# Kernel optimization log

Hardware: AMD Instinct MI355X
Metric: run time of the kernel (lower is better)

The kernel has to match this reference:

```python
import jax, jax.numpy as jnp
import numpy as np

B, S, DMODEL, NHEAD = 2, 2048, 1024, 16
DK = DMODEL // NHEAD
INITRANGE = 0.1


def setup_inputs() -> dict:
    key = jax.random.key(0)
    kq, kk, kv, kwq, kwk, kwv, kwo = jax.random.split(key, 7)
    unif = lambda k, shape: jax.random.uniform(k, shape, jnp.float32, -INITRANGE, INITRANGE)
    return {
        "Q": jax.random.normal(kq, (B, S, DMODEL), jnp.float32),
        "K": jax.random.normal(kk, (B, S, DMODEL), jnp.float32),
        "V": jax.random.normal(kv, (B, S, DMODEL), jnp.float32),
        "WQ": unif(kwq, (NHEAD, DMODEL, DK)),
        "WK": unif(kwk, (NHEAD, DMODEL, DK)),
        "WV": unif(kwv, (NHEAD, DMODEL, DK)),
        "WO": unif(kwo, (NHEAD * DK, DMODEL)),
    }


def reference(Q, K, V, WQ, WK, WV, WO):
    dk = WQ.shape[-1]
    # per-head projections: [B,S,D] x [H,D,dk] -> [B,H,S,dk]
    Qi = jnp.einsum('bsd,hdk->bhsk', Q, WQ)
    Ki = jnp.einsum('bsd,hdk->bhsk', K, WK)
    Vi = jnp.einsum('bsd,hdk->bhsk', V, WV)
    scale = 1.0 / jnp.sqrt(jnp.asarray(dk, Qi.dtype))
    # full attention matrix [B,H,S,S] (faithful to the hand-rolled module; dropout in eval mode)
    attn = jax.nn.softmax(jnp.einsum('bhsk,bhtk->bhst', Qi, Ki) * scale, axis=-1)
    headi = jnp.einsum('bhst,bhtk->bhsk', attn, Vi)  # [B,H,S,dk]
    b, h, s, _ = headi.shape
    # NOTE: original does a raw reshape of contiguous (B,H,S,dk) -> (B,S,H*dk),
    # which mixes head and sequence axes in memory order. jnp row-major reshape
    # reproduces exactly the same element layout.
    out = headi.reshape(b, s, h * dk) @ WO  # [B,S,DMODEL]
    return out
```

## Files before the change

### kernel.cpp

```cpp
#include <hip/hip_runtime.h>
#include <hip/hip_bf16.h>
#include <stdint.h>

typedef unsigned short u16;
typedef unsigned int u32;
typedef __attribute__((ext_vector_type(4))) float f32x4;
typedef __attribute__((ext_vector_type(16))) float f32x16;
typedef __attribute__((ext_vector_type(8))) short bf16x8;
typedef __attribute__((ext_vector_type(4))) unsigned int u32x4;
typedef __attribute__((ext_vector_type(2))) unsigned int u32x2;

#define DEV __device__ __forceinline__

DEV u16 f2bf(float f) {
  union { float f; uint32_t u; } v; v.f = f;
  uint32_t u = v.u;
  return (u16)((u + 0x7fffu + ((u >> 16) & 1u)) >> 16);
}
DEV float bf2f(u16 h) {
  union { uint32_t u; float f; } v; v.u = ((uint32_t)h) << 16;
  return v.f;
}

DEV u32 cvtpk(float a, float b) {
  u32 r;
  asm("v_cvt_pk_bf16_f32 %0, %1, %2" : "=v"(r) : "v"(a), "v"(b));
  return r;
}

DEV void plswap(u32& a, u32& b) {
  asm("v_permlane32_swap_b32 %0, %1" : "+v"(a), "+v"(b));
}

DEV float fexp2(float x) {
  float r;
  asm("v_exp_f32 %0, %1" : "=v"(r) : "v"(x));
  return r;
}

DEV void gload_lds16(const u16* g, u16* l) {
  __builtin_amdgcn_global_load_lds(
      (const __attribute__((address_space(1))) void*)g,
      (__attribute__((address_space(3))) void*)l, 16, 0, 0);
}

__global__ __launch_bounds__(256) void prep_tw_kernel(
    const float* __restrict__ Q, const float* __restrict__ K, const float* __restrict__ V,
    const float* __restrict__ WQ, const float* __restrict__ WK, const float* __restrict__ WV,
    const float* __restrict__ WO,
    u16* __restrict__ Qb, u16* __restrict__ Kb, u16* __restrict__ Vb,
    u16* __restrict__ Wt, u16* __restrict__ Wot) {
  __shared__ __align__(16) u16 tl[64][72];
  const int tid = threadIdx.x;
  if (blockIdx.x < 4096) {
    const int i = blockIdx.x * 256 + tid;
#pragma unroll
    for (int it = 0; it < 3; ++it) {
      int idx = it * 1048576 + i;
      int which = idx >> 20, j = idx & 1048575;
      const float* src = which == 0 ? Q : (which == 1 ? K : V);
      u16* dst = which == 0 ? Qb : (which == 1 ? Kb : Vb);
      float4 v = ((const float4*)src)[j];
      u32x2 pk;
      pk[0] = (u32)f2bf(v.x) | ((u32)f2bf(v.y) << 16);
      pk[1] = (u32)f2bf(v.z) | ((u32)f2bf(v.w) << 16);
      *(u32x2*)(dst + (size_t)j * 4) = pk;
    }
    return;
  }
  const int bid = blockIdx.x - 4096;
  const float* src;
  u16* dst;
  int rstride;
  if (bid < 768) {
    int p = bid >> 8, rest = bid & 255;
    int h = rest >> 4, dt = rest & 15;
    const float* W = p == 0 ? WQ : (p == 1 ? WK : WV);
    src = W + (size_t)(h * 1024 + dt * 64) * 64;
    dst = Wt + (size_t)p * 1048576 + (size_t)h * 64 * 1024 + dt * 64;
    rstride = 64;
  } else {
    int idx2 = bid - 768;
    int kt = idx2 >> 4, ct = idx2 & 15;
    src = WO + (size_t)kt * 64 * 1024 + ct * 64;
    dst = Wot + (size_t)ct * 64 * 1024 + kt * 64;
    rstride = 1024;
  }
#pragma unroll
  for (int i = 0; i < 2; ++i) {
    int idx = i * 256 + tid;
    int row = idx >> 3, c8 = idx & 7;
    const float* sp = src + (size_t)row * rstride + c8 * 8;
    float4 a = *(const float4*)sp;
    float4 b = *(const float4*)(sp + 4);
    u32x4 pk;
    pk[0] = (u32)f2bf(a.x) | ((u32)f2bf(a.y) << 16);
    pk[1] = (u32)f2bf(a.z) | ((u32)f2bf(a.w) << 16);
    pk[2] = (u32)f2bf(b.x) | ((u32)f2bf(b.y) << 16);
    pk[3] = (u32)f2bf(b.z) | ((u32)f2bf(b.w) << 16);
    *(u32x4*)&tl[row][c8 * 8] = pk;
  }
  __syncthreads();
#pragma unroll
  for (int i = 0; i < 2; ++i) {
    int idx = i * 256 + tid;
    int row2 = idx >> 3, s8 = idx & 7;
    u32x4 outv;
    u16* tp = (u16*)&outv;
#pragma unroll
    for (int j = 0; j < 8; ++j) tp[j] = tl[s8 * 8 + j][row2];
    *(u32x4*)(dst + (size_t)row2 * 1024 + s8 * 8) = outv;
  }
}

template <int OUT_BF16>
__global__ __launch_bounds__(256, 3) void gemm_kernel(const u16* __restrict__ A,
                                                      const u16* __restrict__ Bt,
                                                      void* __restrict__ Cout,
                                                      u16* __restrict__ VtOut) {
  __shared__ __align__(16) u16 Alds[128 * 64];
  __shared__ __align__(16) u16 Blds[128 * 64];
  const size_t zo = blockIdx.z;
  A += zo * 4194304;
  Bt += zo * 1048576;
  const int tid = threadIdx.x;
  const int l = tid & 63, w = tid >> 6;
  const int wm = w >> 1, wn = w & 1;
  const int d = blockIdx.x + 32 * blockIdx.y;
  const int orig = (d & 7) * 32 + (d >> 3);
  const int tileM = (orig & 31) * 128, tileN = (orig >> 5) * 128;
  const int lr = l >> 3, lch = l & 7;

  f32x4 acc[4][4] = {};

  for (int kt = 0; kt < 16; ++kt) {
    const int k0 = kt * 64;
#pragma unroll
    for (int i = 0; i < 4; ++i) {
      int r = i * 32 + w * 8 + lr;
      int sch = lch ^ (r & 7);
      gload_lds16(A + (size_t)(tileM + r) * 1024 + k0 + sch * 8, Alds + i * 2048 + w * 512);
      gload_lds16(Bt + (size_t)(tileN + r) * 1024 + k0 + sch * 8, Blds + i * 2048 + w * 512);
    }
    __syncthreads();
    bf16x8 af[4][2], bfr[4][2];
#pragma unroll
    for (int m = 0; m < 4; ++m) {
#pragma unroll
      for (int kk = 0; kk < 2; ++kk) {
        int row = wm * 64 + m * 16 + (l & 15);
        int ch = ((l >> 4) + kk * 4) ^ (row & 7);
        af[m][kk] = *(const bf16x8*)(Alds + row * 64 + ch * 8);
        int rowb = wn * 64 + m * 16 + (l & 15);
        int chb = ((l >> 4) + kk * 4) ^ (rowb & 7);
        bfr[m][kk] = *(const bf16x8*)(Blds + rowb * 64 + chb * 8);
      }
    }
#pragma unroll
    for (int m = 0; m < 4; ++m)
#pragma unroll
      for (int n = 0; n < 4; ++n)
#pragma unroll
        for (int kk = 0; kk < 2; ++kk)
          acc[m][n] = __builtin_amdgcn_mfma_f32_16x16x32_bf16(af[m][kk], bfr[n][kk], acc[m][n], 0, 0, 0);
    __syncthreads();
  }
#pragma unroll
  for (int m = 0; m < 4; ++m) {
    int row0 = tileM + wm * 64 + m * 16 + ((l >> 4) << 2);
#pragma unroll
    for (int n = 0; n < 4; ++n) {
      int col = tileN + wn * 64 + n * 16 + (l & 15);
#pragma unroll
      for (int q = 0; q < 4; ++q) {
        if (OUT_BF16) {
          u16 val = f2bf(acc[m][n][q]);
          if (zo == 2) {
            int g = row0 + q;
            int bq = g >> 11, s = g & 2047;
            int hh = col >> 6, dk = col & 63;
            VtOut[((((size_t)bq << 4) + hh) * 64 + dk) * 2048 + s] = val;
          } else {
            ((u16*)Cout)[zo * 4194304 + (size_t)(row0 + q) * 1024 + col] = val;
          }
        } else {
          ((float*)Cout)[(size_t)(row0 + q) * 1024 + col] = acc[m][n][q];
        }
      }
    }
  }
}

__global__ __launch_bounds__(256, 4) void attn_kernel(const u16* __restrict__ Qi,
                                                      const u16* __restrict__ Ki,
                                                      const u16* __restrict__ Vt,
                                                      u16* __restrict__ Op,
                                                      float* __restrict__ Lp) {
  __shared__ __align__(16) u16 Kl[2][4096];
  __shared__ __align__(16) u16 Vl[2][4096];
  const int tid = threadIdx.x;
  const int l = tid & 63, w = tid >> 6;
  const int lq = l & 31, hi = l >> 5;
  const int lr = l >> 3, lch = l & 7;
  const int dd = blockIdx.x;
  const int orig = (dd & 7) * 128 + (dd >> 3);
  const int bh = orig >> 5;
  const int rem = orig & 31;
  const int qb = rem >> 1, kvh = rem & 1;
  const int b = bh >> 4, h = bh & 15;
  const int qt = qb * 128 + w * 32;
  const int tb = kvh * 1024;

  const u16* Kbase = Ki + (size_t)b * 2048 * 1024 + h * 64;
  const u16* Vbase = Vt + (size_t)bh * 64 * 2048;

  bf16x8 qf[4];
  {
    const u16* qp = Qi + (size_t)(b * 2048 + qt + lq) * 1024 + h * 64 + hi * 8;
#pragma unroll
    for (int s = 0; s < 4; ++s) {
      u32x4 t4 = *(const u32x4*)(qp + s * 16);
      u16* tp = (u16*)&t4;
#pragma unroll
      for (int j = 0; j < 8; ++j) tp[j] = f2bf(bf2f(tp[j]) * 0.1803368867f);
      qf[s] = *(bf16x8*)&t4;
    }
  }

  f32x16 o0 = {}, o1 = {};
  float l_r = 0.f;

  auto STAGE = [&](int bb, int t) {
#pragma unroll
    for (int i = 0; i < 2; ++i) {
      int r = i * 32 + w * 8 + lr;
      int sch = lch ^ (r & 7);
      gload_lds16(Kbase + (size_t)(tb + t * 64 + r) * 1024 + sch * 8,
                  Kl[bb] + i * 2048 + w * 512);
      gload_lds16(Vbase + (size_t)r * 2048 + tb + t * 64 + sch * 8,
                  Vl[bb] + i * 2048 + w * 512);
    }
  };

  STAGE(0, 0);

#pragma unroll 2
  for (int tile = 0; tile < 16; ++tile) {
    const int cur = tile & 1;
    __syncthreads();
    if (tile + 1 < 16) STAGE(cur ^ 1, tile + 1);
    const u16* kl = Kl[cur];
    const u16* vl = Vl[cur];

    f32x16 s0 = {}, s1 = {};
    __builtin_amdgcn_s_setprio(1);
#pragma unroll
    for (int s = 0; s < 4; ++s) {
      int row = lq, c = s * 2 + hi;
      bf16x8 kf = *(const bf16x8*)(kl + row * 64 + (c ^ (row & 7)) * 8);
      s0 = __builtin_amdgcn_mfma_f32_32x32x16_bf16(kf, qf[s], s0, 0, 0, 0);
    }
#pragma unroll
    for (int s = 0; s < 4; ++s) {
      int row = 32 + lq, c = s * 2 + hi;
      bf16x8 kf = *(const bf16x8*)(kl + row * 64 + (c ^ (row & 7)) * 8);
      s1 = __builtin_amdgcn_mfma_f32_32x32x16_bf16(kf, qf[s], s1, 0, 0, 0);
    }
    __builtin_amdgcn_s_setprio(0);

    float rs = 0.f;
    bf16x8 pa[4];
#pragma unroll
    for (int s4 = 0; s4 < 4; ++s4) {
      const int rb = 8 * (s4 & 1);
      float p[8];
#pragma unroll
      for (int j = 0; j < 8; ++j) {
        float sv = (s4 < 2) ? ((const float*)&s0)[rb + j] : ((const float*)&s1)[rb + j];
        p[j] = fexp2(sv);
      }
      rs += ((p[0] + p[1]) + (p[2] + p[3])) + ((p[4] + p[5]) + (p[6] + p[7]));
      u32 w10 = cvtpk(p[0], p[1]);
      u32 w11 = cvtpk(p[2], p[3]);
      u32 w20 = cvtpk(p[4], p[5]);
      u32 w21 = cvtpk(p[6], p[7]);
      plswap(w10, w20);
      plswap(w11, w21);
      u32x4 af;
      af[0] = w10;
      af[1] = w11;
      af[2] = w20;
      af[3] = w21;
      pa[s4] = *(bf16x8*)&af;
    }
    rs += __shfl_xor(rs, 32, 64);
    l_r += rs;

    __builtin_amdgcn_s_setprio(1);
#pragma unroll
    for (int s4 = 0; s4 < 4; ++s4) {
      int rowd = lq, c = s4 * 2 + hi;
      bf16x8 vf = *(const bf16x8*)(vl + rowd * 64 + (c ^ (rowd & 7)) * 8);
      o0 = __builtin_amdgcn_mfma_f32_32x32x16_bf16(pa[s4], vf, o0, 0, 0, 0);
    }
#pragma unroll
    for (int s4 = 0; s4 < 4; ++s4) {
      int rowd = 32 + lq, c = s4 * 2 + hi;
      bf16x8 vf = *(const bf16x8*)(vl + rowd * 64 + (c ^ (rowd & 7)) * 8);
      o1 = __builtin_amdgcn_mfma_f32_32x32x16_bf16(pa[s4], vf, o1, 0, 0, 0);
    }
    __builtin_amdgcn_s_setprio(0);
  }

#pragma unroll
  for (int r = 0; r < 16; ++r) {
    int qr = (r & 3) + 8 * (r >> 2) + 4 * hi;
    u16* hp = Op + (size_t)kvh * 4194304 + ((size_t)bh * 2048 + qt + qr) * 64;
    hp[lq] = f2bf(o0[r]);
    hp[32 + lq] = f2bf(o1[r]);
  }
  if (hi == 0) Lp[(size_t)kvh * 65536 + (size_t)bh * 2048 + qt + lq] = l_r;
}

__global__ __launch_bounds__(256) void combine_kernel(const u16* __restrict__ Op,
                                                      const float* __restrict__ Lp,
                                                      u16* __restrict__ Hd) {
  const int idx = blockIdx.x * 256 + threadIdx.x;
  const int g = idx >> 3, j = idx & 7;
  const float fac = 1.f / (Lp[g] + Lp[65536 + g]);
  const size_t off = (size_t)g * 64 + j * 8;
  u32x4 va = *(const u32x4*)(Op + off);
  u32x4 vb = *(const u32x4*)(Op + 4194304 + off);
  const u16* pa = (const u16*)&va;
  const u16* pb = (const u16*)&vb;
  u32x4 outv;
  u16* po = (u16*)&outv;
#pragma unroll
  for (int e = 0; e < 8; ++e) po[e] = f2bf((bf2f(pa[e]) + bf2f(pb[e])) * fac);
  *(u32x4*)(Hd + off) = outv;
}

extern "C" void kernel_launch(void* const* d_in, const int* in_sizes, int n_in,
                              void* d_out, int out_size, void* d_ws, size_t ws_size,
                              hipStream_t stream) {
  const float* Q = (const float*)d_in[0];
  const float* K = (const float*)d_in[1];
  const float* V = (const float*)d_in[2];
  const float* WQ = (const float*)d_in[3];
  const float* WK = (const float*)d_in[4];
  const float* WV = (const float*)d_in[5];
  const float* WO = (const float*)d_in[6];
  float* out = (float*)d_out;

  size_t off = 0;
  char* ws = (char*)d_ws;
  auto nxt = [&](size_t n) { void* p = ws + off; off += (n + 255) & ~(size_t)255; return p; };
  u16* Qb = (u16*)nxt(3ull * 4096 * 1024 * 2);
  u16* Qi = (u16*)nxt(3ull * 4096 * 1024 * 2);
  u16* Vtb = (u16*)nxt(4096ull * 1024 * 2);
  u16* Hd = (u16*)nxt(4096ull * 1024 * 2);
  u16* Wt = (u16*)nxt(3ull * 1048576 * 2);
  u16* Wot = (u16*)nxt(1048576ull * 2);
  float* Lp = (float*)nxt(2ull * 65536 * 4);
  u16* Ki = Qi + 4194304;
  u16* Op = Qb;

  prep_tw_kernel<<<5120, 256, 0, stream>>>(Q, K, V, WQ, WK, WV, WO, Qb, Qb + 4194304,
                                           Qb + 2 * 4194304, Wt, Wot);

  gemm_kernel<1><<<dim3(32, 8, 3), 256, 0, stream>>>(Qb, Wt, Qi, Vtb);

  attn_kernel<<<1024, 256, 0, stream>>>(Qi, Ki, Vtb, Op, Lp);

  combine_kernel<<<2048, 256, 0, stream>>>(Op, Lp, Hd);

  gemm_kernel<0><<<dim3(32, 8, 1), 256, 0, stream>>>(Hd, Wot, out, nullptr);
}
```

Before: 133.0 us.

## Fuse fp32-to-bf16 input conversion into projection GEMM and compute row sums via MFMA

Drops the separate pass that converts Q/K/V to bf16. The projection GEMM now reads fp32 activations directly, converts them in registers and stores them to LDS, which saves a full read and write of the bf16 copies. The tile order is changed to M-major ordering for the projection, and the transpose kernel now uses packed conversions. In attention, the softmax row sum is moved from VALU adds plus a shuffle into an extra MFMA against a vector of ones, which adds matrix work and loses the async global-to-LDS load for A in the projection.

```diff
diff --git a/kernel.cpp b/kernel.cpp
--- a/kernel.cpp
+++ b/kernel.cpp
@@ -44,31 +44,12 @@
       (__attribute__((address_space(3))) void*)l, 16, 0, 0);
 }
 
-__global__ __launch_bounds__(256) void prep_tw_kernel(
-    const float* __restrict__ Q, const float* __restrict__ K, const float* __restrict__ V,
+__global__ __launch_bounds__(256) void transposeW_kernel(
     const float* __restrict__ WQ, const float* __restrict__ WK, const float* __restrict__ WV,
-    const float* __restrict__ WO,
-    u16* __restrict__ Qb, u16* __restrict__ Kb, u16* __restrict__ Vb,
-    u16* __restrict__ Wt, u16* __restrict__ Wot) {
+    const float* __restrict__ WO, u16* __restrict__ Wt, u16* __restrict__ Wot) {
   __shared__ __align__(16) u16 tl[64][72];
   const int tid = threadIdx.x;
-  if (blockIdx.x < 4096) {
-    const int i = blockIdx.x * 256 + tid;
-#pragma unroll
-    for (int it = 0; it < 3; ++it) {
-      int idx = it * 1048576 + i;
-      int which = idx >> 20, j = idx & 1048575;
-      const float* src = which == 0 ? Q : (which == 1 ? K : V);
-      u16* dst = which == 0 ? Qb : (which == 1 ? Kb : Vb);
-      float4 v = ((const float4*)src)[j];
-      u32x2 pk;
-      pk[0] = (u32)f2bf(v.x) | ((u32)f2bf(v.y) << 16);
-      pk[1] = (u32)f2bf(v.z) | ((u32)f2bf(v.w) << 16);
-      *(u32x2*)(dst + (size_t)j * 4) = pk;
-    }
-    return;
-  }
-  const int bid = blockIdx.x - 4096;
+  const int bid = blockIdx.x;
   const float* src;
   u16* dst;
   int rstride;
@@ -94,10 +75,10 @@
     float4 a = *(const float4*)sp;
     float4 b = *(const float4*)(sp + 4);
     u32x4 pk;
-    pk[0] = (u32)f2bf(a.x) | ((u32)f2bf(a.y) << 16);
-    pk[1] = (u32)f2bf(a.z) | ((u32)f2bf(a.w) << 16);
-    pk[2] = (u32)f2bf(b.x) | ((u32)f2bf(b.y) << 16);
-    pk[3] = (u32)f2bf(b.z) | ((u32)f2bf(b.w) << 16);
+    pk[0] = cvtpk(a.x, a.y);
+    pk[1] = cvtpk(a.z, a.w);
+    pk[2] = cvtpk(b.x, b.y);
+    pk[3] = cvtpk(b.z, b.w);
     *(u32x4*)&tl[row][c8 * 8] = pk;
   }
   __syncthreads();
@@ -114,21 +95,21 @@
 }
 
 template <int OUT_BF16>
-__global__ __launch_bounds__(256, 3) void gemm_kernel(const u16* __restrict__ A,
-                                                      const u16* __restrict__ Bt,
-                                                      void* __restrict__ Cout,
-                                                      u16* __restrict__ VtOut) {
+__global__ __launch_bounds__(256, 3) void gemm_kernel(
+    const float* __restrict__ F0, const float* __restrict__ F1, const float* __restrict__ F2,
+    const u16* __restrict__ Abf, const u16* __restrict__ Bt,
+    void* __restrict__ Cout, u16* __restrict__ VtOut) {
   __shared__ __align__(16) u16 Alds[128 * 64];
   __shared__ __align__(16) u16 Blds[128 * 64];
   const size_t zo = blockIdx.z;
-  A += zo * 4194304;
+  const float* Af = zo == 0 ? F0 : (zo == 1 ? F1 : F2);
   Bt += zo * 1048576;
   const int tid = threadIdx.x;
   const int l = tid & 63, w = tid >> 6;
   const int wm = w >> 1, wn = w & 1;
   const int d = blockIdx.x + 32 * blockIdx.y;
   const int orig = (d & 7) * 32 + (d >> 3);
-  const int tileM = (orig & 31) * 128, tileN = (orig >> 5) * 128;
+  const int tileM = (orig >> 3) * 128, tileN = (orig & 7) * 128;
   const int lr = l >> 3, lch = l & 7;
 
   f32x4 acc[4][4] = {};
@@ -139,7 +120,20 @@
     for (int i = 0; i < 4; ++i) {
       int r = i * 32 + w * 8 + lr;
       int sch = lch ^ (r & 7);
-      gload_lds16(A + (size_t)(tileM + r) * 1024 + k0 + sch * 8, Alds + i * 2048 + w * 512);
+      if (OUT_BF16) {
+        const float* sp = Af + (size_t)(tileM + r) * 1024 + k0 + sch * 8;
+        float4 a = *(const float4*)sp;
+        float4 b = *(const float4*)(sp + 4);
+        u32x4 pk;
+        pk[0] = cvtpk(a.x, a.y);
+        pk[1] = cvtpk(a.z, a.w);
+        pk[2] = cvtpk(b.x, b.y);
+        pk[3] = cvtpk(b.z, b.w);
+        *(u32x4*)(Alds + i * 2048 + w * 512 + l * 8) = pk;
+      } else {
+        gload_lds16(Abf + (size_t)(tileM + r) * 1024 + k0 + sch * 8,
+                    Alds + i * 2048 + w * 512);
+      }
       gload_lds16(Bt + (size_t)(tileN + r) * 1024 + k0 + sch * 8, Blds + i * 2048 + w * 512);
     }
     __syncthreads();
@@ -227,8 +221,14 @@
     }
   }
 
-  f32x16 o0 = {}, o1 = {};
-  float l_r = 0.f;
+  bf16x8 ones;
+  {
+    u32x4 ov;
+    ov[0] = ov[1] = ov[2] = ov[3] = 0x3F803F80u;
+    ones = *(bf16x8*)&ov;
+  }
+
+  f32x16 o0 = {}, o1 = {}, lacc = {};
 
   auto STAGE = [&](int bb, int t) {
 #pragma unroll
@@ -268,7 +268,6 @@
     }
     __builtin_amdgcn_s_setprio(0);
 
-    float rs = 0.f;
     bf16x8 pa[4];
 #pragma unroll
     for (int s4 = 0; s4 < 4; ++s4) {
@@ -279,7 +278,6 @@
         float sv = (s4 < 2) ? ((const float*)&s0)[rb + j] : ((const float*)&s1)[rb + j];
         p[j] = fexp2(sv);
       }
-      rs += ((p[0] + p[1]) + (p[2] + p[3])) + ((p[4] + p[5]) + (p[6] + p[7]));
       u32 w10 = cvtpk(p[0], p[1]);
       u32 w11 = cvtpk(p[2], p[3]);
       u32 w20 = cvtpk(p[4], p[5]);
@@ -293,8 +291,6 @@
       af[3] = w21;
       pa[s4] = *(bf16x8*)&af;
     }
-    rs += __shfl_xor(rs, 32, 64);
-    l_r += rs;
 
     __builtin_amdgcn_s_setprio(1);
 #pragma unroll
@@ -309,6 +305,9 @@
       bf16x8 vf = *(const bf16x8*)(vl + rowd * 64 + (c ^ (rowd & 7)) * 8);
       o1 = __builtin_amdgcn_mfma_f32_32x32x16_bf16(pa[s4], vf, o1, 0, 0, 0);
     }
+#pragma unroll
+    for (int s4 = 0; s4 < 4; ++s4)
+      lacc = __builtin_amdgcn_mfma_f32_32x32x16_bf16(pa[s4], ones, lacc, 0, 0, 0);
     __builtin_amdgcn_s_setprio(0);
   }
 
@@ -319,7 +318,13 @@
     hp[lq] = f2bf(o0[r]);
     hp[32 + lq] = f2bf(o1[r]);
   }
-  if (hi == 0) Lp[(size_t)kvh * 65536 + (size_t)bh * 2048 + qt + lq] = l_r;
+  if (lq == 0) {
+#pragma unroll
+    for (int r = 0; r < 16; ++r) {
+      int qr = (r & 3) + 8 * (r >> 2) + 4 * hi;
+      Lp[(size_t)kvh * 65536 + (size_t)bh * 2048 + qt + qr] = lacc[r];
+    }
+  }
 }
 
 __global__ __launch_bounds__(256) void combine_kernel(const u16* __restrict__ Op,
@@ -355,24 +360,22 @@
   size_t off = 0;
   char* ws = (char*)d_ws;
   auto nxt = [&](size_t n) { void* p = ws + off; off += (n + 255) & ~(size_t)255; return p; };
-  u16* Qb = (u16*)nxt(3ull * 4096 * 1024 * 2);
   u16* Qi = (u16*)nxt(3ull * 4096 * 1024 * 2);
   u16* Vtb = (u16*)nxt(4096ull * 1024 * 2);
   u16* Hd = (u16*)nxt(4096ull * 1024 * 2);
   u16* Wt = (u16*)nxt(3ull * 1048576 * 2);
   u16* Wot = (u16*)nxt(1048576ull * 2);
   float* Lp = (float*)nxt(2ull * 65536 * 4);
+  u16* Op = (u16*)nxt(2ull * 4194304 * 2);
   u16* Ki = Qi + 4194304;
-  u16* Op = Qb;
-
-  prep_tw_kernel<<<5120, 256, 0, stream>>>(Q, K, V, WQ, WK, WV, WO, Qb, Qb + 4194304,
-                                           Qb + 2 * 4194304, Wt, Wot);
-
-  gemm_kernel<1><<<dim3(32, 8, 3), 256, 0, stream>>>(Qb, Wt, Qi, Vtb);
+
+  transposeW_kernel<<<1024, 256, 0, stream>>>(WQ, WK, WV, WO, Wt, Wot);
+
+  gemm_kernel<1><<<dim3(32, 8, 3), 256, 0, stream>>>(Q, K, V, nullptr, Wt, Qi, Vtb);
 
   attn_kernel<<<1024, 256, 0, stream>>>(Qi, Ki, Vtb, Op, Lp);
 
   combine_kernel<<<2048, 256, 0, stream>>>(Op, Lp, Hd);
 
-  gemm_kernel<0><<<dim3(32, 8, 1), 256, 0, stream>>>(Hd, Wot, out, nullptr);
-}
+  gemm_kernel<0><<<dim3(32, 8, 1), 256, 0, stream>>>(nullptr, nullptr, nullptr, Hd, Wot, out, nullptr);
+}
```

After: 139.9 us. +5.2%, slower.
